# Performance work log

Hardware: AMD Instinct MI355X
Metric: run time of the kernel (lower is better)

Reference implementation:

```python
import jax, jax.numpy as jnp
import numpy as np

N, L, S, H, D = 2, 4096, 4096, 8, 64


def setup_inputs() -> dict:
    key = jax.random.key(0)
    kq, kk, kv = jax.random.split(key, 3)
    queries = jax.random.normal(kq, (N, L, H, D), dtype=jnp.float32)
    keys = jax.random.normal(kk, (N, S, H, D), dtype=jnp.float32)
    values = jax.random.normal(kv, (N, S, H, D), dtype=jnp.float32)
    return {"queries": queries, "keys": keys, "values": values}


def reference(queries, keys, values):
    # Full (non-fused) scaled dot-product attention, LoFTR FullAttention.
    # QK: [N, L, S, H]
    softmax_temp = 1.0 / jnp.sqrt(jnp.asarray(queries.shape[3], queries.dtype))
    QK = jnp.einsum('nlhd,nshd->nlsh', queries, keys)
    A = jax.nn.softmax(softmax_temp * QK, axis=2)  # softmax over S
    out = jnp.einsum('nlsh,nshd->nlhd', A, values)  # [N, L, H, D]
    return out
```

## Files before the change

kernel.cpp:

```cpp
#include <hip/hip_runtime.h>
#include <hip/hip_bf16.h>

typedef float  f32x4  __attribute__((ext_vector_type(4)));
typedef float  f32x16 __attribute__((ext_vector_type(16)));
typedef short  short8 __attribute__((ext_vector_type(8)));
typedef int    i32x2  __attribute__((ext_vector_type(2)));
typedef unsigned int uint4v __attribute__((ext_vector_type(4)));

#define N_  2
#define L_  4096
#define S_  4096
#define H_  8
#define D_  64
#define HD_ 512
#define KVB 64
#define QB  128
#define NTL 32

__device__ __forceinline__ unsigned short f2bf(float f) {
  unsigned int u = __builtin_bit_cast(unsigned int, f);
  u += 0x7fffu + ((u >> 16) & 1u);
  return (unsigned short)(u >> 16);
}
__device__ __forceinline__ unsigned short bf16c(float f) {
  return __builtin_bit_cast(unsigned short, __float2bfloat16(f));
}
__device__ __forceinline__ unsigned int pk2(float lo, float hi) {
  unsigned int r;
  asm("v_cvt_pk_bf16_f32 %0, %1, %2" : "=v"(r) : "v"(lo), "v"(hi));
  return r;
}
__device__ __forceinline__ f32x16 zero16() {
  f32x16 v;
  #pragma unroll
  for (int i = 0; i < 16; ++i) v[i] = 0.f;
  return v;
}
__device__ __forceinline__ float tsum16(const f32x16& v) {
  float a0 = v[0] + v[1],   a1 = v[2] + v[3];
  float a2 = v[4] + v[5],   a3 = v[6] + v[7];
  float a4 = v[8] + v[9],   a5 = v[10] + v[11];
  float a6 = v[12] + v[13], a7 = v[14] + v[15];
  float b0 = a0 + a1, b1 = a2 + a3, b2 = a4 + a5, b3 = a6 + a7;
  return (b0 + b1) + (b2 + b3);
}

#define GLD16(gp, lp)                                                          \
  __builtin_amdgcn_global_load_lds(                                            \
      (const __attribute__((address_space(1))) unsigned int*)(gp),             \
      (__attribute__((address_space(3))) unsigned int*)(lp), 16, 0, 0)

__global__ __launch_bounds__(256, 8)
void prepack(const float* __restrict__ Kg, const float* __restrict__ Vg,
             unsigned short* __restrict__ Kw, unsigned short* __restrict__ Vw) {
  const int b = blockIdx.x;
  const int tid = threadIdx.x;
  const int isV = (b >= 1024);
  const int tb = isV ? b - 1024 : b;
  const int nh = tb >> 6, t = tb & 63;
  const int n = nh >> 3, h = nh & 7;

  if (!isV) {
    const int sl = tid >> 2, d0 = (tid & 3) << 4;
    const float* src = Kg + ((size_t)(n * S_ + t * 64 + sl) * H_ + h) * D_ + d0;
    f32x4 x0 = *(const f32x4*)(src);
    f32x4 x1 = *(const f32x4*)(src + 4);
    f32x4 x2 = *(const f32x4*)(src + 8);
    f32x4 x3 = *(const f32x4*)(src + 12);
    short8 t0, t1;
    t0[0] = (short)f2bf(x0[0]); t0[1] = (short)f2bf(x0[1]);
    t0[2] = (short)f2bf(x0[2]); t0[3] = (short)f2bf(x0[3]);
    t0[4] = (short)f2bf(x1[0]); t0[5] = (short)f2bf(x1[1]);
    t0[6] = (short)f2bf(x1[2]); t0[7] = (short)f2bf(x1[3]);
    t1[0] = (short)f2bf(x2[0]); t1[1] = (short)f2bf(x2[1]);
    t1[2] = (short)f2bf(x2[2]); t1[3] = (short)f2bf(x2[3]);
    t1[4] = (short)f2bf(x3[0]); t1[5] = (short)f2bf(x3[1]);
    t1[6] = (short)f2bf(x3[2]); t1[7] = (short)f2bf(x3[3]);
    unsigned short* dst = Kw + (size_t)tb * 4096 + sl * 64;
    const int b0 = d0 >> 3;
    *(short8*)&dst[((b0)     ^ (sl & 7)) * 8] = t0;
    *(short8*)&dst[((b0 + 1) ^ (sl & 7)) * 8] = t1;
  } else {
    const int d = tid & 63, sb2 = tid >> 6;
    #pragma unroll
    for (int c = 0; c < 2; ++c) {
      const int sblk = sb2 * 2 + c;
      const float* src = Vg + ((size_t)(n * S_ + t * 64 + sblk * 8) * H_ + h) * D_ + d;
      short8 o;
      #pragma unroll
      for (int j = 0; j < 8; ++j) o[j] = (short)f2bf(src[(size_t)j * HD_]);
      *(short8*)&Vw[(size_t)tb * 4096 + sblk * 512 + d * 8] = o;
    }
  }
}

template<int W1, int W2, int DOK, int DOV>
__device__ __forceinline__ void tile_body(
    int t, const int hi, const int c32, const int qw,
    const char* Kth, const char* Vth, const size_t klane, const size_t vlane,
    unsigned short (*Klh)[KVB * D_],
    const short8 qf[4], const short8* vc, short8* vn,
    f32x16& acc0, f32x16& acc1, float& lsum)
{
  const int cur = t & 1;
  asm volatile("s_waitcnt vmcnt(%0)" :: "n"(W1) : "memory");
  __builtin_amdgcn_s_barrier();
  const unsigned short* Kb = Klh[cur];

  short8 kf0[4], kf1[4];
  #pragma unroll
  for (int kc = 0; kc < 4; ++kc) {
    const int ph = (((kc << 1) | hi) ^ (c32 & 7)) * 8;
    kf0[kc] = *(const short8*)&Kb[c32 * 64 + ph];
    kf1[kc] = *(const short8*)&Kb[(32 + c32) * 64 + ph];
  }

  f32x16 s0a = zero16(), s1a = zero16();
  __builtin_amdgcn_s_setprio(1);
  #pragma unroll
  for (int kc = 0; kc < 4; ++kc) {
    s0a = __builtin_amdgcn_mfma_f32_32x32x16_bf16(kf0[kc], qf[kc], s0a, 0, 0, 0);
    s1a = __builtin_amdgcn_mfma_f32_32x32x16_bf16(kf1[kc], qf[kc], s1a, 0, 0, 0);
  }
  __builtin_amdgcn_s_setprio(0);

  asm volatile("s_waitcnt lgkmcnt(0)" ::: "memory");
  __builtin_amdgcn_s_barrier();

  if (DOK) {
    const char* kp = Kth + (size_t)(t + 2) * 8192 + klane;
    GLD16(kp,        &Klh[cur][qw << 9]);
    GLD16(kp + 4096, &Klh[cur][2048 + (qw << 9)]);
  }
  if (DOV) {
    const char* vp = Vth + (size_t)(t + 1) * 8192 + vlane;
    #pragma unroll
    for (int q8 = 0; q8 < 8; ++q8)
      vn[q8] = *(const short8*)(vp + (q8 >> 1) * 2048 + (q8 & 1) * 512);
  }

  #pragma unroll
  for (int r = 0; r < 16; ++r) s0a[r] = __builtin_amdgcn_exp2f(s0a[r]);
  #pragma unroll
  for (int r = 0; r < 16; ++r) s1a[r] = __builtin_amdgcn_exp2f(s1a[r]);
  lsum += tsum16(s0a) + tsum16(s1a);

  asm volatile("s_waitcnt vmcnt(%0)" :: "n"(W2) : "memory");
  __builtin_amdgcn_sched_barrier(0);

  #pragma unroll
  for (int sc = 0; sc < 4; ++sc) {
    const int c = sc & 1;
    unsigned int c0, c1, c2, c3;
    if (sc < 2) {
      c0 = pk2(s0a[8 * c + 0], s0a[8 * c + 1]);
      c1 = pk2(s0a[8 * c + 2], s0a[8 * c + 3]);
      c2 = pk2(s0a[8 * c + 4], s0a[8 * c + 5]);
      c3 = pk2(s0a[8 * c + 6], s0a[8 * c + 7]);
    } else {
      c0 = pk2(s1a[8 * c + 0], s1a[8 * c + 1]);
      c1 = pk2(s1a[8 * c + 2], s1a[8 * c + 3]);
      c2 = pk2(s1a[8 * c + 4], s1a[8 * c + 5]);
      c3 = pk2(s1a[8 * c + 6], s1a[8 * c + 7]);
    }
    i32x2 r0 = __builtin_amdgcn_permlane32_swap((int)c0, (int)c2, false, false);
    i32x2 r1 = __builtin_amdgcn_permlane32_swap((int)c1, (int)c3, false, false);
    uint4v w = { (unsigned)r0[0], (unsigned)r1[0], (unsigned)r0[1], (unsigned)r1[1] };
    const short8 pa = __builtin_bit_cast(short8, w);
    __builtin_amdgcn_s_setprio(1);
    acc0 = __builtin_amdgcn_mfma_f32_32x32x16_bf16(pa, vc[sc * 2 + 0], acc0, 0, 0, 0);
    acc1 = __builtin_amdgcn_mfma_f32_32x32x16_bf16(pa, vc[sc * 2 + 1], acc1, 0, 0, 0);
    __builtin_amdgcn_s_setprio(0);
  }
}

__global__ __launch_bounds__(512, 2)
void attn_fa5(const float* __restrict__ Qg,
              const unsigned short* __restrict__ Kw,
              const unsigned short* __restrict__ Vw,
              float* __restrict__ Og) {
  __shared__ __align__(16) unsigned short Kl[2][2][KVB * D_];
  __shared__ float CombL[4][32];

  const int tid = threadIdx.x;
  const int wv  = tid >> 6;
  const int qw  = wv & 3;
  const int sh  = wv >> 2;
  const int ln  = tid & 63;
  const int hi  = ln >> 5;
  const int c32 = ln & 31;

  const int bid = blockIdx.x;
  const int swz = (bid & 7) * 64 + (bid >> 3);
  const int qt  = swz & 31;
  const int nh  = swz >> 5;
  const int h = nh & 7, n = nh >> 3;
  const int qbase = qt * QB;

  const float qs = 0.125f * 1.44269504088896340736f;
  const int qrow = qbase + (qw << 5) + c32;
  const float* qp = Qg + (size_t)(n * L_ + qrow) * HD_ + h * D_ + (hi << 3);
  short8 qf[4];
  #pragma unroll
  for (int kc = 0; kc < 4; ++kc) {
    const float* p = qp + (kc << 4);
    f32x4 a = *(const f32x4*)(p);
    f32x4 b = *(const f32x4*)(p + 4);
    short8 f;
    f[0] = (short)bf16c(a[0] * qs); f[1] = (short)bf16c(a[1] * qs);
    f[2] = (short)bf16c(a[2] * qs); f[3] = (short)bf16c(a[3] * qs);
    f[4] = (short)bf16c(b[0] * qs); f[5] = (short)bf16c(b[1] * qs);
    f[6] = (short)bf16c(b[2] * qs); f[7] = (short)bf16c(b[3] * qs);
    qf[kc] = f;
  }
  asm volatile("s_waitcnt vmcnt(0)" ::: "memory");

  f32x16 acc0 = zero16(), acc1 = zero16();
  float lsum = 0.f;

  const char* Kth = (const char*)(Kw + (size_t)nh * 64 * 4096) + (size_t)sh * NTL * 8192;
  const char* Vth = (const char*)(Vw + (size_t)nh * 64 * 4096) + (size_t)sh * NTL * 8192;
  const size_t klane = (size_t)((qw << 10) + (ln << 4));
  const size_t vlane = (size_t)((hi << 10) + (c32 << 4));
  unsigned short (*Klh)[KVB * D_] = Kl[sh];

  short8 vA[8], vB[8];

  GLD16(Kth + klane,               &Klh[0][qw << 9]);
  GLD16(Kth + klane + 4096,        &Klh[0][2048 + (qw << 9)]);
  GLD16(Kth + 8192 + klane,        &Klh[1][qw << 9]);
  GLD16(Kth + 8192 + klane + 4096, &Klh[1][2048 + (qw << 9)]);
  {
    const char* vp = Vth + vlane;
    #pragma unroll
    for (int q8 = 0; q8 < 8; ++q8)
      vA[q8] = *(const short8*)(vp + (q8 >> 1) * 2048 + (q8 & 1) * 512);
  }

  for (int t = 0; t < NTL - 2; t += 2) {
    tile_body<10, 10, 1, 1>(t,     hi, c32, qw, Kth, Vth, klane, vlane, Klh, qf, vA, vB, acc0, acc1, lsum);
    tile_body<10, 10, 1, 1>(t + 1, hi, c32, qw, Kth, Vth, klane, vlane, Klh, qf, vB, vA, acc0, acc1, lsum);
  }
  tile_body<10, 8, 0, 1>(NTL - 2, hi, c32, qw, Kth, Vth, klane, vlane, Klh, qf, vA, vB, acc0, acc1, lsum);
  tile_body< 8, 0, 0, 0>(NTL - 1, hi, c32, qw, Kth, Vth, klane, vlane, Klh, qf, vB, vA, acc0, acc1, lsum);

  const float full = lsum + __shfl_xor(lsum, 32);
  float* C = (float*)&Kl[0][0][0] + (size_t)qw * 2048;

  if (sh == 1) {
    #pragma unroll
    for (int r = 0; r < 16; ++r) {
      const int q = (r & 3) + 8 * (r >> 2) + 4 * hi;
      C[q * 64 + c32]      = acc0[r];
      C[q * 64 + 32 + c32] = acc1[r];
    }
    if (hi == 0) CombL[qw][c32] = full;
  }
  __syncthreads();
  if (sh == 0) {
    const float ltot = full + CombL[qw][c32];
    #pragma unroll
    for (int r = 0; r < 16; ++r) {
      const int q = (r & 3) + 8 * (r >> 2) + 4 * hi;
      const float l = __shfl(ltot, q);
      const float inv = 1.f / l;
      const int row = qbase + (qw << 5) + q;
      float* op = Og + (size_t)(n * L_ + row) * HD_ + h * D_ + c32;
      op[0]  = (acc0[r] + C[q * 64 + c32]) * inv;
      op[32] = (acc1[r] + C[q * 64 + 32 + c32]) * inv;
    }
  }
}

extern "C" void kernel_launch(void* const* d_in, const int* in_sizes, int n_in,
                              void* d_out, int out_size, void* d_ws, size_t ws_size,
                              hipStream_t stream) {
  (void)in_sizes; (void)n_in; (void)out_size; (void)ws_size;
  const float* Q = (const float*)d_in[0];
  const float* K = (const float*)d_in[1];
  const float* V = (const float*)d_in[2];
  float* O = (float*)d_out;

  unsigned short* Kw = (unsigned short*)d_ws;
  unsigned short* Vw = Kw + 4194304;
  hipLaunchKernelGGL(prepack, dim3(2048), dim3(256), 0, stream, K, V, Kw, Vw);
  hipLaunchKernelGGL(attn_fa5, dim3(512), dim3(512), 0, stream, Q, Kw, Vw, O);
}
```

Baseline: 105.7 us.

## Load K fragments directly from global into registers, drop LDS staging and barriers

Prepack now writes K in a fragment-ready layout, so each lane can load its MFMA operand straight from global memory instead of going through LDS via global_load_lds. This removes the LDS K buffers and the per-tile block barriers. The tile body is also split into two half-tiles, so the K loads for the next tile overlap the exp/PV work of the current one. The trade-off is more register pressure and more global/L2 traffic, because the waves of a block no longer share K through LDS; every wave now re-reads the same K.

```diff
diff --git a/kernel.cpp b/kernel.cpp
--- a/kernel.cpp
+++ b/kernel.cpp
@@ -44,11 +44,6 @@
   float b0 = a0 + a1, b1 = a2 + a3, b2 = a4 + a5, b3 = a6 + a7;
   return (b0 + b1) + (b2 + b3);
 }
-
-#define GLD16(gp, lp)                                                          \
-  __builtin_amdgcn_global_load_lds(                                            \
-      (const __attribute__((address_space(1))) unsigned int*)(gp),             \
-      (__attribute__((address_space(3))) unsigned int*)(lp), 16, 0, 0)
 
 __global__ __launch_bounds__(256, 8)
 void prepack(const float* __restrict__ Kg, const float* __restrict__ Vg,
@@ -76,10 +71,10 @@
     t1[2] = (short)f2bf(x2[2]); t1[3] = (short)f2bf(x2[3]);
     t1[4] = (short)f2bf(x3[0]); t1[5] = (short)f2bf(x3[1]);
     t1[6] = (short)f2bf(x3[2]); t1[7] = (short)f2bf(x3[3]);
-    unsigned short* dst = Kw + (size_t)tb * 4096 + sl * 64;
+    unsigned short* dst = Kw + (size_t)tb * 4096;
     const int b0 = d0 >> 3;
-    *(short8*)&dst[((b0)     ^ (sl & 7)) * 8] = t0;
-    *(short8*)&dst[((b0 + 1) ^ (sl & 7)) * 8] = t1;
+    *(short8*)&dst[(b0)     * 512 + sl * 8] = t0;
+    *(short8*)&dst[(b0 + 1) * 512 + sl * 8] = t1;
   } else {
     const int d = tid & 63, sb2 = tid >> 6;
     #pragma unroll
@@ -94,92 +89,100 @@
   }
 }
 
-template<int W1, int W2, int DOK, int DOV>
+template<int W1, int Wa, int Wb, int DOK, int DOV>
 __device__ __forceinline__ void tile_body(
-    int t, const int hi, const int c32, const int qw,
-    const char* Kth, const char* Vth, const size_t klane, const size_t vlane,
-    unsigned short (*Klh)[KVB * D_],
-    const short8 qf[4], const short8* vc, short8* vn,
+    int t, const char* kbase, const char* vbase,
+    const short8 qf[4], short8 kf0[4], short8 kf1[4], short8 vf[8],
     f32x16& acc0, f32x16& acc1, float& lsum)
 {
-  const int cur = t & 1;
   asm volatile("s_waitcnt vmcnt(%0)" :: "n"(W1) : "memory");
-  __builtin_amdgcn_s_barrier();
-  const unsigned short* Kb = Klh[cur];
-
-  short8 kf0[4], kf1[4];
-  #pragma unroll
-  for (int kc = 0; kc < 4; ++kc) {
-    const int ph = (((kc << 1) | hi) ^ (c32 & 7)) * 8;
-    kf0[kc] = *(const short8*)&Kb[c32 * 64 + ph];
-    kf1[kc] = *(const short8*)&Kb[(32 + c32) * 64 + ph];
-  }
-
-  f32x16 s0a = zero16(), s1a = zero16();
+  __builtin_amdgcn_sched_barrier(0);
+  f32x16 s0a = zero16();
   __builtin_amdgcn_s_setprio(1);
   #pragma unroll
-  for (int kc = 0; kc < 4; ++kc) {
+  for (int kc = 0; kc < 4; ++kc)
     s0a = __builtin_amdgcn_mfma_f32_32x32x16_bf16(kf0[kc], qf[kc], s0a, 0, 0, 0);
-    s1a = __builtin_amdgcn_mfma_f32_32x32x16_bf16(kf1[kc], qf[kc], s1a, 0, 0, 0);
-  }
   __builtin_amdgcn_s_setprio(0);
 
-  asm volatile("s_waitcnt lgkmcnt(0)" ::: "memory");
-  __builtin_amdgcn_s_barrier();
-
   if (DOK) {
-    const char* kp = Kth + (size_t)(t + 2) * 8192 + klane;
-    GLD16(kp,        &Klh[cur][qw << 9]);
-    GLD16(kp + 4096, &Klh[cur][2048 + (qw << 9)]);
-  }
-  if (DOV) {
-    const char* vp = Vth + (size_t)(t + 1) * 8192 + vlane;
-    #pragma unroll
-    for (int q8 = 0; q8 < 8; ++q8)
-      vn[q8] = *(const short8*)(vp + (q8 >> 1) * 2048 + (q8 & 1) * 512);
+    const char* kp = kbase + (size_t)(t + 1) * 8192;
+    #pragma unroll
+    for (int kc = 0; kc < 4; ++kc)
+      kf0[kc] = *(const short8*)(kp + kc * 2048);
   }
 
   #pragma unroll
   for (int r = 0; r < 16; ++r) s0a[r] = __builtin_amdgcn_exp2f(s0a[r]);
-  #pragma unroll
-  for (int r = 0; r < 16; ++r) s1a[r] = __builtin_amdgcn_exp2f(s1a[r]);
-  lsum += tsum16(s0a) + tsum16(s1a);
-
-  asm volatile("s_waitcnt vmcnt(%0)" :: "n"(W2) : "memory");
+  lsum += tsum16(s0a);
+
+  asm volatile("s_waitcnt vmcnt(%0)" :: "n"(Wa) : "memory");
   __builtin_amdgcn_sched_barrier(0);
-
-  #pragma unroll
-  for (int sc = 0; sc < 4; ++sc) {
-    const int c = sc & 1;
-    unsigned int c0, c1, c2, c3;
-    if (sc < 2) {
-      c0 = pk2(s0a[8 * c + 0], s0a[8 * c + 1]);
-      c1 = pk2(s0a[8 * c + 2], s0a[8 * c + 3]);
-      c2 = pk2(s0a[8 * c + 4], s0a[8 * c + 5]);
-      c3 = pk2(s0a[8 * c + 6], s0a[8 * c + 7]);
-    } else {
-      c0 = pk2(s1a[8 * c + 0], s1a[8 * c + 1]);
-      c1 = pk2(s1a[8 * c + 2], s1a[8 * c + 3]);
-      c2 = pk2(s1a[8 * c + 4], s1a[8 * c + 5]);
-      c3 = pk2(s1a[8 * c + 6], s1a[8 * c + 7]);
-    }
+  #pragma unroll
+  for (int sc = 0; sc < 2; ++sc) {
+    const unsigned int c0 = pk2(s0a[8 * sc + 0], s0a[8 * sc + 1]);
+    const unsigned int c1 = pk2(s0a[8 * sc + 2], s0a[8 * sc + 3]);
+    const unsigned int c2 = pk2(s0a[8 * sc + 4], s0a[8 * sc + 5]);
+    const unsigned int c3 = pk2(s0a[8 * sc + 6], s0a[8 * sc + 7]);
     i32x2 r0 = __builtin_amdgcn_permlane32_swap((int)c0, (int)c2, false, false);
     i32x2 r1 = __builtin_amdgcn_permlane32_swap((int)c1, (int)c3, false, false);
     uint4v w = { (unsigned)r0[0], (unsigned)r1[0], (unsigned)r0[1], (unsigned)r1[1] };
     const short8 pa = __builtin_bit_cast(short8, w);
     __builtin_amdgcn_s_setprio(1);
-    acc0 = __builtin_amdgcn_mfma_f32_32x32x16_bf16(pa, vc[sc * 2 + 0], acc0, 0, 0, 0);
-    acc1 = __builtin_amdgcn_mfma_f32_32x32x16_bf16(pa, vc[sc * 2 + 1], acc1, 0, 0, 0);
+    acc0 = __builtin_amdgcn_mfma_f32_32x32x16_bf16(pa, vf[sc * 2 + 0], acc0, 0, 0, 0);
+    acc1 = __builtin_amdgcn_mfma_f32_32x32x16_bf16(pa, vf[sc * 2 + 1], acc1, 0, 0, 0);
     __builtin_amdgcn_s_setprio(0);
   }
+
+  f32x16 s1a = zero16();
+  __builtin_amdgcn_s_setprio(1);
+  #pragma unroll
+  for (int kc = 0; kc < 4; ++kc)
+    s1a = __builtin_amdgcn_mfma_f32_32x32x16_bf16(kf1[kc], qf[kc], s1a, 0, 0, 0);
+  __builtin_amdgcn_s_setprio(0);
+
+  if (DOK) {
+    const char* kp = kbase + (size_t)(t + 1) * 8192 + 512;
+    #pragma unroll
+    for (int kc = 0; kc < 4; ++kc)
+      kf1[kc] = *(const short8*)(kp + kc * 2048);
+  }
+
+  #pragma unroll
+  for (int r = 0; r < 16; ++r) s1a[r] = __builtin_amdgcn_exp2f(s1a[r]);
+  lsum += tsum16(s1a);
+
+  asm volatile("s_waitcnt vmcnt(%0)" :: "n"(Wb) : "memory");
+  __builtin_amdgcn_sched_barrier(0);
+  #pragma unroll
+  for (int sc = 0; sc < 2; ++sc) {
+    const unsigned int c0 = pk2(s1a[8 * sc + 0], s1a[8 * sc + 1]);
+    const unsigned int c1 = pk2(s1a[8 * sc + 2], s1a[8 * sc + 3]);
+    const unsigned int c2 = pk2(s1a[8 * sc + 4], s1a[8 * sc + 5]);
+    const unsigned int c3 = pk2(s1a[8 * sc + 6], s1a[8 * sc + 7]);
+    i32x2 r0 = __builtin_amdgcn_permlane32_swap((int)c0, (int)c2, false, false);
+    i32x2 r1 = __builtin_amdgcn_permlane32_swap((int)c1, (int)c3, false, false);
+    uint4v w = { (unsigned)r0[0], (unsigned)r1[0], (unsigned)r0[1], (unsigned)r1[1] };
+    const short8 pa = __builtin_bit_cast(short8, w);
+    __builtin_amdgcn_s_setprio(1);
+    acc0 = __builtin_amdgcn_mfma_f32_32x32x16_bf16(pa, vf[4 + sc * 2 + 0], acc0, 0, 0, 0);
+    acc1 = __builtin_amdgcn_mfma_f32_32x32x16_bf16(pa, vf[4 + sc * 2 + 1], acc1, 0, 0, 0);
+    __builtin_amdgcn_s_setprio(0);
+  }
+
+  if (DOV) {
+    const char* vp = vbase + (size_t)(t + 1) * 8192;
+    #pragma unroll
+    for (int q8 = 0; q8 < 8; ++q8)
+      vf[q8] = *(const short8*)(vp + (q8 >> 1) * 2048 + (q8 & 1) * 512);
+  }
 }
 
 __global__ __launch_bounds__(512, 2)
-void attn_fa5(const float* __restrict__ Qg,
+void attn_fa6(const float* __restrict__ Qg,
               const unsigned short* __restrict__ Kw,
               const unsigned short* __restrict__ Vw,
               float* __restrict__ Og) {
-  __shared__ __align__(16) unsigned short Kl[2][2][KVB * D_];
+  __shared__ __align__(16) float Comb[4][2048];
   __shared__ float CombL[4][32];
 
   const int tid = threadIdx.x;
@@ -218,34 +221,28 @@
   f32x16 acc0 = zero16(), acc1 = zero16();
   float lsum = 0.f;
 
-  const char* Kth = (const char*)(Kw + (size_t)nh * 64 * 4096) + (size_t)sh * NTL * 8192;
-  const char* Vth = (const char*)(Vw + (size_t)nh * 64 * 4096) + (size_t)sh * NTL * 8192;
-  const size_t klane = (size_t)((qw << 10) + (ln << 4));
-  const size_t vlane = (size_t)((hi << 10) + (c32 << 4));
-  unsigned short (*Klh)[KVB * D_] = Kl[sh];
-
-  short8 vA[8], vB[8];
-
-  GLD16(Kth + klane,               &Klh[0][qw << 9]);
-  GLD16(Kth + klane + 4096,        &Klh[0][2048 + (qw << 9)]);
-  GLD16(Kth + 8192 + klane,        &Klh[1][qw << 9]);
-  GLD16(Kth + 8192 + klane + 4096, &Klh[1][2048 + (qw << 9)]);
-  {
-    const char* vp = Vth + vlane;
-    #pragma unroll
-    for (int q8 = 0; q8 < 8; ++q8)
-      vA[q8] = *(const short8*)(vp + (q8 >> 1) * 2048 + (q8 & 1) * 512);
-  }
-
-  for (int t = 0; t < NTL - 2; t += 2) {
-    tile_body<10, 10, 1, 1>(t,     hi, c32, qw, Kth, Vth, klane, vlane, Klh, qf, vA, vB, acc0, acc1, lsum);
-    tile_body<10, 10, 1, 1>(t + 1, hi, c32, qw, Kth, Vth, klane, vlane, Klh, qf, vB, vA, acc0, acc1, lsum);
-  }
-  tile_body<10, 8, 0, 1>(NTL - 2, hi, c32, qw, Kth, Vth, klane, vlane, Klh, qf, vA, vB, acc0, acc1, lsum);
-  tile_body< 8, 0, 0, 0>(NTL - 1, hi, c32, qw, Kth, Vth, klane, vlane, Klh, qf, vB, vA, acc0, acc1, lsum);
+  const char* kbase = (const char*)(Kw + (size_t)nh * 64 * 4096)
+                      + (size_t)sh * NTL * 8192 + (hi << 10) + (c32 << 4);
+  const char* vbase = (const char*)(Vw + (size_t)nh * 64 * 4096)
+                      + (size_t)sh * NTL * 8192 + (hi << 10) + (c32 << 4);
+
+  short8 kf0[4], kf1[4], vf[8];
+
+  #pragma unroll
+  for (int kc = 0; kc < 4; ++kc) {
+    kf0[kc] = *(const short8*)(kbase + kc * 2048);
+    kf1[kc] = *(const short8*)(kbase + kc * 2048 + 512);
+  }
+  #pragma unroll
+  for (int q8 = 0; q8 < 8; ++q8)
+    vf[q8] = *(const short8*)(vbase + (q8 >> 1) * 2048 + (q8 & 1) * 512);
+
+  for (int t = 0; t < NTL - 1; ++t)
+    tile_body<8, 8, 8, 1, 1>(t, kbase, vbase, qf, kf0, kf1, vf, acc0, acc1, lsum);
+  tile_body<8, 4, 0, 0, 0>(NTL - 1, kbase, vbase, qf, kf0, kf1, vf, acc0, acc1, lsum);
 
   const float full = lsum + __shfl_xor(lsum, 32);
-  float* C = (float*)&Kl[0][0][0] + (size_t)qw * 2048;
+  float* C = &Comb[qw][0];
 
   if (sh == 1) {
     #pragma unroll
@@ -284,5 +281,5 @@
   unsigned short* Kw = (unsigned short*)d_ws;
   unsigned short* Vw = Kw + 4194304;
   hipLaunchKernelGGL(prepack, dim3(2048), dim3(256), 0, stream, K, V, Kw, Vw);
-  hipLaunchKernelGGL(attn_fa5, dim3(512), dim3(512), 0, stream, Q, Kw, Vw, O);
-}
+  hipLaunchKernelGGL(attn_fa6, dim3(512), dim3(512), 0, stream, Q, Kw, Vw, O);
+}
```

Result: faster. 100.4 us (-5.1%).
